# Kernel optimization log

Measured on AMD Instinct MI355X. Metric: run time of the kernel, lower is better.

## Reference

```python
import jax, jax.numpy as jnp
import numpy as np

# MLA (multi-head latent attention) config
DIM = 1024
HEADS = 16
DIM_HEAD = DIM // HEADS          # 64
LATENT = DIM // 4                # 256, compressed KV latent dim
SCALE = DIM_HEAD ** -0.5


def setup_inputs() -> dict:
    key = jax.random.key(0)
    ks = jax.random.split(key, 8)
    B, S = 2, 2048
    init = lambda k, shape, fan_in: jax.random.normal(k, shape, jnp.float32) * (fan_in ** -0.5)
    return {
        "x":  jax.random.normal(ks[0], (B, S, DIM), jnp.float32),
        "Wq": init(ks[1], (DIM, DIM), DIM),
        "bq": jnp.zeros((DIM,), jnp.float32),
        "Wl": init(ks[2], (DIM, LATENT), DIM),      # down-projection to compressed KV latent
        "bl": jnp.zeros((LATENT,), jnp.float32),
        "Wk": init(ks[3], (LATENT, DIM), LATENT),   # latent -> per-head keys
        "bk": jnp.zeros((DIM,), jnp.float32),
        "Wv": init(ks[4], (LATENT, DIM), LATENT),   # latent -> per-head values
        "bv": jnp.zeros((DIM,), jnp.float32),
        "Wo": init(ks[5], (DIM, DIM), DIM),         # Attention.to_out
        "bo": jnp.zeros((DIM,), jnp.float32),
    }


def reference(x, Wq, bq, Wl, bl, Wk, bk, Wv, bv, Wo, bo):
    B, S, D = x.shape
    H, Dh = HEADS, DIM_HEAD
    # query projection
    q = (x @ Wq + bq).reshape(B, S, H, Dh)
    # compressed KV latent (this is what would be cached; kv_cache=None here)
    latent = x @ Wl + bl                              # [B, S, LATENT]
    k = (latent @ Wk + bk).reshape(B, S, H, Dh)
    v = (latent @ Wv + bv).reshape(B, S, H, Dh)
    # attention
    scores = jnp.einsum('bihd,bjhd->bhij', q, k) * SCALE   # [B, H, S, S]
    attn = jax.nn.softmax(scores, axis=-1)
    out = jnp.einsum('bhij,bjhd->bihd', attn, v).reshape(B, S, D)
    # dropout(p=0) is identity; output projection
    out = out @ Wo + bo
    return out
```

## Files before the change

kernel.cpp:

```cpp
#include <hip/hip_runtime.h>


typedef _Float16 half8  __attribute__((ext_vector_type(8)));
typedef _Float16 half4  __attribute__((ext_vector_type(4)));
typedef float    floatx4 __attribute__((ext_vector_type(4)));

__global__ __launch_bounds__(256) void prep(
    const float* __restrict__ x,
    const float* __restrict__ Wq, const float* __restrict__ Wl,
    const float* __restrict__ Wk, const float* __restrict__ Wv,
    const float* __restrict__ Wo,
    _Float16* __restrict__ xh,
    _Float16* __restrict__ Bt1, _Float16* __restrict__ Bt2,
    _Float16* __restrict__ Wot)
{
    const int t = threadIdx.x;
    if (blockIdx.z == 5) {
        size_t base = ((size_t)(blockIdx.y * 32 + blockIdx.x) * 256 + t) * 16;
#pragma unroll
        for (int it = 0; it < 4; ++it) {
            floatx4 v = *(const floatx4*)(x + base + it * 4);
            *(half4*)(xh + base + it * 4) = __builtin_convertvector(v, half4);
        }
        return;
    }
    const float* src; _Float16* dst; int K, N;
    switch (blockIdx.z) {
        case 0:  src = Wq; dst = Bt1;                 K = 1024; N = 1024; break;
        case 1:  src = Wl; dst = Bt1 + 1024 * 1024;   K = 1024; N = 256;  break;
        case 2:  src = Wk; dst = Bt2;                 K = 256;  N = 1024; break;
        case 3:  src = Wv; dst = Bt2 + 1024 * 256;    K = 256;  N = 1024; break;
        default: src = Wo; dst = Wot;                 K = 1024; N = 1024; break;
    }
    const int n0 = blockIdx.x * 32, k0 = blockIdx.y * 32;
    if (n0 >= N || k0 >= K) return;
    __shared__ _Float16 tile[32][33];
    const int tx = t & 31, ty = t >> 5;
#pragma unroll
    for (int i = 0; i < 4; ++i)
        tile[ty + 8 * i][tx] = (_Float16)src[(size_t)(k0 + ty + 8 * i) * N + n0 + tx];
    __syncthreads();
#pragma unroll
    for (int i = 0; i < 4; ++i)
        dst[(size_t)(n0 + ty + 8 * i) * K + k0 + tx] = tile[tx][ty + 8 * i];
}

template <int MODE>
__global__ __launch_bounds__(256, 4) void gemm_fused(
    const _Float16* __restrict__ A, const _Float16* __restrict__ Bt,
    const float* __restrict__ bias0, const float* __restrict__ bias1,
    void* __restrict__ out0, void* __restrict__ out1,
    const _Float16* __restrict__ O1, const float* __restrict__ lp,
    int N, int K)
{
    __shared__ _Float16 As[128 * 32];
    __shared__ _Float16 Bs[64 * 32];
    __shared__ _Float16 Tt[(MODE == 1) ? 64 * 136 : 1];
    const int t = threadIdx.x;
    const int lane = t & 63, w = t >> 6;
    const int quad = lane >> 4, low = lane & 15;
    const int row0 = blockIdx.y * 128, col0 = blockIdx.x * 64;
    const int wm = (w >> 1) * 64, wn = (w & 1) * 32;

    floatx4 acc[4][2];
    const floatx4 z4 = {0.f, 0.f, 0.f, 0.f};
#pragma unroll
    for (int i = 0; i < 4; ++i)
#pragma unroll
        for (int j = 0; j < 2; ++j) acc[i][j] = z4;

    const int srow = lane >> 2;
    const int scol = (lane & 3) * 8;

    for (int k0 = 0; k0 < K; k0 += 32) {
        __syncthreads();
        if (MODE == 2) {
            const int head = k0 >> 6;
#pragma unroll
            for (int c = 0; c < 2; ++c) {
                const int chunk = w * 2 + c;
                const int row = row0 + chunk * 16 + srow;
                const int li = ((row >> 11) * 16 + head) * 2048 + (row & 2047);
                const float linv = 1.f / (lp[li] + lp[65536 + li]);
                const size_t gi = (size_t)row * 1024 + k0 + scol;
                half8 o0 = *(const half8*)(A + gi);
                half8 o1 = *(const half8*)(O1 + gi);
                half8 sm;
#pragma unroll
                for (int r = 0; r < 8; ++r)
                    sm[r] = (_Float16)(((float)o0[r] + (float)o1[r]) * linv);
                *(half8*)(As + chunk * 512 + lane * 8) = sm;
            }
        } else {
#pragma unroll
            for (int c = 0; c < 2; ++c) {
                const int chunk = w * 2 + c;
                const _Float16* g = A + (size_t)(row0 + chunk * 16 + srow) * K + k0 + scol;
                __builtin_amdgcn_global_load_lds(
                    (const __attribute__((address_space(1))) void*)g,
                    (__attribute__((address_space(3))) void*)(As + chunk * 512), 16, 0, 0);
            }
        }
        {
            const _Float16* g = Bt + (size_t)(col0 + w * 16 + srow) * K + k0 + scol;
            __builtin_amdgcn_global_load_lds(
                (const __attribute__((address_space(1))) void*)g,
                (__attribute__((address_space(3))) void*)(Bs + w * 512), 16, 0, 0);
        }
        __syncthreads();

        half8 a[4], b[2];
#pragma unroll
        for (int i = 0; i < 4; ++i)
            a[i] = *(const half8*)(As + (wm + i * 16 + low) * 32 + quad * 8);
#pragma unroll
        for (int j = 0; j < 2; ++j)
            b[j] = *(const half8*)(Bs + (wn + j * 16 + low) * 32 + quad * 8);
#pragma unroll
        for (int i = 0; i < 4; ++i)
#pragma unroll
            for (int j = 0; j < 2; ++j)
                acc[i][j] = __builtin_amdgcn_mfma_f32_16x16x32_f16(a[i], b[j], acc[i][j], 0, 0, 0);
    }

    if (MODE == 1 && col0 >= 1024) {
        const int hh = (col0 - 1024) >> 6;
        const int bb = row0 >> 11;
        const int tok0 = row0 & 2047;
#pragma unroll
        for (int i = 0; i < 4; ++i)
#pragma unroll
            for (int j = 0; j < 2; ++j) {
                const int lc = wn + j * 16 + low;
                float bv = bias1[hh * 64 + lc];
                half4 ph;
#pragma unroll
                for (int r = 0; r < 4; ++r) ph[r] = (_Float16)(acc[i][j][r] + bv);
                *(half4*)(&Tt[lc * 136 + wm + i * 16 + quad * 4]) = ph;
            }
        __syncthreads();
        _Float16* vb = (_Float16*)out1 + ((size_t)(bb * 16 + hh) * 64) * 2048;
#pragma unroll
        for (int it = 0; it < 4; ++it) {
            const int e = t + 256 * it;
            const int d = e >> 4, tk = (e & 15) * 8;
            half8 val = *(const half8*)(&Tt[d * 136 + tk]);
            *(half8*)(vb + (size_t)d * 2048 + tok0 + tk) = val;
        }
        return;
    }

#pragma unroll
    for (int i = 0; i < 4; ++i) {
#pragma unroll
        for (int j = 0; j < 2; ++j) {
            const int col = col0 + wn + j * 16 + low;
            const int rbase = row0 + wm + i * 16 + quad * 4;
            if (MODE == 2) {
                const float bv = bias0[col];
#pragma unroll
                for (int r = 0; r < 4; ++r)
                    ((float*)out0)[(size_t)(rbase + r) * 1024 + col] = acc[i][j][r] + bv;
            } else if (col < 1024) {
                float bv = bias0[col];
#pragma unroll
                for (int r = 0; r < 4; ++r) {
                    float val = acc[i][j][r] + bv;
                    if (MODE == 0) val *= 0.125f;
                    ((_Float16*)out0)[(size_t)(rbase + r) * 1024 + col] = (_Float16)val;
                }
            } else {
                const int c2 = col - 1024;
                float bv = bias1[c2];
#pragma unroll
                for (int r = 0; r < 4; ++r)
                    ((_Float16*)out1)[(size_t)(rbase + r) * 256 + c2] =
                        (_Float16)(acc[i][j][r] + bv);
            }
        }
    }
}

__global__ __launch_bounds__(256, 2) void mla_attn(
    const _Float16* __restrict__ qp,
    const _Float16* __restrict__ kk,
    const _Float16* __restrict__ vt,
    _Float16* __restrict__ Op0, _Float16* __restrict__ Op1,
    float* __restrict__ lp)
{
    constexpr int S = 2048;
    __shared__ _Float16 Ks[64][76];
    __shared__ _Float16 Vs[64][76];
    __shared__ _Float16 Ps[256][76];

    const int t = threadIdx.x, lane = t & 63, w = t >> 6;
    const int quad = lane >> 4, low = lane & 15;
    const int q0 = blockIdx.x * 256;
    const int b = blockIdx.y >> 4, h = blockIdx.y & 15;
    const int split = blockIdx.z;

    half8 qf[4][2];
#pragma unroll
    for (int ni = 0; ni < 4; ++ni)
#pragma unroll
        for (int ks = 0; ks < 2; ++ks)
            qf[ni][ks] = *(const half8*)(qp +
                (size_t)(b * S + q0 + w * 64 + ni * 16 + low) * 1024 +
                h * 64 + ks * 32 + quad * 8);

    floatx4 oa[4][4], ls[4];
    const floatx4 z4 = {0.f, 0.f, 0.f, 0.f};
#pragma unroll
    for (int mi = 0; mi < 4; ++mi) {
        ls[mi] = z4;
#pragma unroll
        for (int nd = 0; nd < 4; ++nd) oa[mi][nd] = z4;
    }

    const _Float16* kbase = kk + (size_t)(b * S) * 1024 + h * 64;
    const _Float16* vbase = vt + (size_t)(b * 16 + h) * 64 * 2048;

    const int jbeg = split * 1024, jend = jbeg + 1024;
    for (int j0 = jbeg; j0 < jend; j0 += 64) {
        __syncthreads();
#pragma unroll
        for (int p = 0; p < 2; ++p) {
            int c = p * 256 + t;
            int r = c >> 3, o8 = (c & 7) * 8;
            *(half8*)(&Ks[r][o8]) = *(const half8*)(kbase + (size_t)(j0 + r) * 1024 + o8);
            *(half8*)(&Vs[r][o8]) = *(const half8*)(vbase + (size_t)r * 2048 + j0 + o8);
        }
        __syncthreads();

        floatx4 s[4][4];
        const floatx4 i4 = {-3.f, -3.f, -3.f, -3.f};
#pragma unroll
        for (int mj = 0; mj < 4; ++mj)
#pragma unroll
            for (int ni = 0; ni < 4; ++ni) s[mj][ni] = i4;
#pragma unroll
        for (int ks = 0; ks < 2; ++ks) {
            half8 af[4];
#pragma unroll
            for (int mj = 0; mj < 4; ++mj)
                af[mj] = *(const half8*)(&Ks[mj * 16 + low][ks * 32 + quad * 8]);
#pragma unroll
            for (int mj = 0; mj < 4; ++mj)
#pragma unroll
                for (int ni = 0; ni < 4; ++ni)
                    s[mj][ni] = __builtin_amdgcn_mfma_f32_16x16x32_f16(af[mj], qf[ni][ks], s[mj][ni], 0, 0, 0);
        }

#pragma unroll
        for (int mj = 0; mj < 4; ++mj)
#pragma unroll
            for (int ni = 0; ni < 4; ++ni) {
                floatx4 pv;
#pragma unroll
                for (int r = 0; r < 4; ++r) pv[r] = __expf(s[mj][ni][r]);
                ls[ni] += pv;
                half4 ph;
#pragma unroll
                for (int r = 0; r < 4; ++r) ph[r] = (_Float16)pv[r];
                *(half4*)(&Ps[w * 64 + ni * 16 + low][mj * 16 + quad * 4]) = ph;
            }

#pragma unroll
        for (int ks = 0; ks < 2; ++ks) {
            half8 pf[4], vf[4];
#pragma unroll
            for (int mi = 0; mi < 4; ++mi)
                pf[mi] = *(const half8*)(&Ps[w * 64 + mi * 16 + low][ks * 32 + quad * 8]);
#pragma unroll
            for (int nd = 0; nd < 4; ++nd)
                vf[nd] = *(const half8*)(&Vs[nd * 16 + low][ks * 32 + quad * 8]);
#pragma unroll
            for (int mi = 0; mi < 4; ++mi)
#pragma unroll
                for (int nd = 0; nd < 4; ++nd)
                    oa[mi][nd] = __builtin_amdgcn_mfma_f32_16x16x32_f16(pf[mi], vf[nd], oa[mi][nd], 0, 0, 0);
        }
    }

#pragma unroll
    for (int ni = 0; ni < 4; ++ni) {
        float l = ls[ni][0] + ls[ni][1] + ls[ni][2] + ls[ni][3];
        l += __shfl_xor(l, 16);
        l += __shfl_xor(l, 32);
        if (quad == 0)
            lp[split * 65536 + (b * 16 + h) * 2048 + q0 + w * 64 + ni * 16 + low] = l;
    }
    _Float16* op = split ? Op1 : Op0;
#pragma unroll
    for (int mi = 0; mi < 4; ++mi)
#pragma unroll
        for (int nd = 0; nd < 4; ++nd)
#pragma unroll
            for (int r = 0; r < 4; ++r)
                op[(size_t)(b * S + q0 + w * 64 + mi * 16 + quad * 4 + r) * 1024 +
                   h * 64 + nd * 16 + low] = (_Float16)oa[mi][nd][r];
}

extern "C" void kernel_launch(void* const* d_in, const int* in_sizes, int n_in,
                              void* d_out, int out_size, void* d_ws, size_t ws_size,
                              hipStream_t stream) {
    const float* x  = (const float*)d_in[0];
    const float* Wq = (const float*)d_in[1];
    const float* bq = (const float*)d_in[2];
    const float* Wl = (const float*)d_in[3];
    const float* bl = (const float*)d_in[4];
    const float* Wk = (const float*)d_in[5];
    const float* bk = (const float*)d_in[6];
    const float* Wv = (const float*)d_in[7];
    const float* bv = (const float*)d_in[8];
    const float* Wo = (const float*)d_in[9];
    const float* bo = (const float*)d_in[10];
    float* out = (float*)d_out;

    _Float16* p   = (_Float16*)d_ws;
    _Float16* xh  = p; p += 4194304;
    _Float16* qh  = p; p += 4194304;
    _Float16* kh  = p; p += 4194304;
    _Float16* vtb = p; p += 4194304;
    _Float16* ah  = p; p += 4194304;
    _Float16* lat = p; p += 1048576;
    _Float16* Bt1 = p; p += 1310720;
    _Float16* Bt2 = p; p += 524288;
    _Float16* Wot = p; p += 1048576;

    prep<<<dim3(32, 32, 6), 256, 0, stream>>>(x, Wq, Wl, Wk, Wv, Wo, xh, Bt1, Bt2, Wot);

    gemm_fused<0><<<dim3(20, 32), 256, 0, stream>>>(
        xh, Bt1, bq, bl, qh, lat, nullptr, nullptr, 1280, 1024);
    gemm_fused<1><<<dim3(32, 32), 256, 0, stream>>>(
        lat, Bt2, bk, bv, kh, vtb, nullptr, nullptr, 2048, 256);
    mla_attn<<<dim3(8, 32, 2), 256, 0, stream>>>(qh, kh, vtb, ah, xh, (float*)lat);
    gemm_fused<2><<<dim3(16, 32), 256, 0, stream>>>(
        ah, Wot, bo, nullptr, out, nullptr, xh, (const float*)lat, 1024, 1024);
}
```

Before: 226.2 us.

## Swizzle GEMM operand layouts in global memory and split attention combine into its own kernel

```diff
diff --git a/kernel.cpp b/kernel.cpp
--- a/kernel.cpp
+++ b/kernel.cpp
@@ -4,6 +4,8 @@
 typedef _Float16 half8  __attribute__((ext_vector_type(8)));
 typedef _Float16 half4  __attribute__((ext_vector_type(4)));
 typedef float    floatx4 __attribute__((ext_vector_type(4)));
+
+__device__ __forceinline__ int swz_mask(int row) { return ((row ^ (row >> 2)) & 3) << 3; }
 
 __global__ __launch_bounds__(256) void prep(
     const float* __restrict__ x,
@@ -16,11 +18,16 @@
 {
     const int t = threadIdx.x;
     if (blockIdx.z == 5) {
-        size_t base = ((size_t)(blockIdx.y * 32 + blockIdx.x) * 256 + t) * 16;
+        size_t gbase = ((size_t)(blockIdx.y * 32 + blockIdx.x) * 256 + t) * 16;
+        const int row = (int)(gbase >> 10);
+        const int m = swz_mask(row);
+        const size_t rowbase = (size_t)row << 10;
+        const int h0 = (int)(gbase & 1023);
 #pragma unroll
         for (int it = 0; it < 4; ++it) {
-            floatx4 v = *(const floatx4*)(x + base + it * 4);
-            *(half4*)(xh + base + it * 4) = __builtin_convertvector(v, half4);
+            floatx4 v = *(const floatx4*)(x + gbase + it * 4);
+            *(half4*)(xh + rowbase + ((h0 + it * 4) ^ m)) =
+                __builtin_convertvector(v, half4);
         }
         return;
     }
@@ -41,8 +48,10 @@
         tile[ty + 8 * i][tx] = (_Float16)src[(size_t)(k0 + ty + 8 * i) * N + n0 + tx];
     __syncthreads();
 #pragma unroll
-    for (int i = 0; i < 4; ++i)
-        dst[(size_t)(n0 + ty + 8 * i) * K + k0 + tx] = tile[tx][ty + 8 * i];
+    for (int i = 0; i < 4; ++i) {
+        const int n = n0 + ty + 8 * i;
+        dst[(size_t)n * K + ((k0 + tx) ^ swz_mask(n))] = tile[tx][ty + 8 * i];
+    }
 }
 
 template <int MODE>
@@ -50,7 +59,6 @@
     const _Float16* __restrict__ A, const _Float16* __restrict__ Bt,
     const float* __restrict__ bias0, const float* __restrict__ bias1,
     void* __restrict__ out0, void* __restrict__ out1,
-    const _Float16* __restrict__ O1, const float* __restrict__ lp,
     int N, int K)
 {
     __shared__ _Float16 As[128 * 32];
@@ -61,6 +69,7 @@
     const int quad = lane >> 4, low = lane & 15;
     const int row0 = blockIdx.y * 128, col0 = blockIdx.x * 64;
     const int wm = (w >> 1) * 64, wn = (w & 1) * 32;
+    const int swz = ((low ^ (low >> 2)) & 3) << 3;
 
     floatx4 acc[4][2];
     const floatx4 z4 = {0.f, 0.f, 0.f, 0.f};
@@ -74,32 +83,13 @@
 
     for (int k0 = 0; k0 < K; k0 += 32) {
         __syncthreads();
-        if (MODE == 2) {
-            const int head = k0 >> 6;
-#pragma unroll
-            for (int c = 0; c < 2; ++c) {
-                const int chunk = w * 2 + c;
-                const int row = row0 + chunk * 16 + srow;
-                const int li = ((row >> 11) * 16 + head) * 2048 + (row & 2047);
-                const float linv = 1.f / (lp[li] + lp[65536 + li]);
-                const size_t gi = (size_t)row * 1024 + k0 + scol;
-                half8 o0 = *(const half8*)(A + gi);
-                half8 o1 = *(const half8*)(O1 + gi);
-                half8 sm;
-#pragma unroll
-                for (int r = 0; r < 8; ++r)
-                    sm[r] = (_Float16)(((float)o0[r] + (float)o1[r]) * linv);
-                *(half8*)(As + chunk * 512 + lane * 8) = sm;
-            }
-        } else {
-#pragma unroll
-            for (int c = 0; c < 2; ++c) {
-                const int chunk = w * 2 + c;
-                const _Float16* g = A + (size_t)(row0 + chunk * 16 + srow) * K + k0 + scol;
-                __builtin_amdgcn_global_load_lds(
-                    (const __attribute__((address_space(1))) void*)g,
-                    (__attribute__((address_space(3))) void*)(As + chunk * 512), 16, 0, 0);
-            }
+#pragma unroll
+        for (int c = 0; c < 2; ++c) {
+            const int chunk = w * 2 + c;
+            const _Float16* g = A + (size_t)(row0 + chunk * 16 + srow) * K + k0 + scol;
+            __builtin_amdgcn_global_load_lds(
+                (const __attribute__((address_space(1))) void*)g,
+                (__attribute__((address_space(3))) void*)(As + chunk * 512), 16, 0, 0);
         }
         {
             const _Float16* g = Bt + (size_t)(col0 + w * 16 + srow) * K + k0 + scol;
@@ -112,10 +102,10 @@
         half8 a[4], b[2];
 #pragma unroll
         for (int i = 0; i < 4; ++i)
-            a[i] = *(const half8*)(As + (wm + i * 16 + low) * 32 + quad * 8);
+            a[i] = *(const half8*)(As + (wm + i * 16 + low) * 32 + ((quad * 8) ^ swz));
 #pragma unroll
         for (int j = 0; j < 2; ++j)
-            b[j] = *(const half8*)(Bs + (wn + j * 16 + low) * 32 + quad * 8);
+            b[j] = *(const half8*)(Bs + (wn + j * 16 + low) * 32 + ((quad * 8) ^ swz));
 #pragma unroll
         for (int i = 0; i < 4; ++i)
 #pragma unroll
@@ -173,9 +163,11 @@
                 const int c2 = col - 1024;
                 float bv = bias1[c2];
 #pragma unroll
-                for (int r = 0; r < 4; ++r)
-                    ((_Float16*)out1)[(size_t)(rbase + r) * 256 + c2] =
+                for (int r = 0; r < 4; ++r) {
+                    const int row = rbase + r;
+                    ((_Float16*)out1)[(size_t)row * 256 + (c2 ^ swz_mask(row))] =
                         (_Float16)(acc[i][j][r] + bv);
+                }
             }
         }
     }
@@ -299,6 +291,24 @@
             for (int r = 0; r < 4; ++r)
                 op[(size_t)(b * S + q0 + w * 64 + mi * 16 + quad * 4 + r) * 1024 +
                    h * 64 + nd * 16 + low] = (_Float16)oa[mi][nd][r];
+}
+
+__global__ __launch_bounds__(256) void attn_combine(
+    const _Float16* __restrict__ O0, const _Float16* __restrict__ O1,
+    const float* __restrict__ lp, _Float16* __restrict__ att)
+{
+    size_t idx = ((size_t)blockIdx.x * 256 + threadIdx.x) * 8;
+    int row = (int)(idx >> 10), c = (int)(idx & 1023);
+    int b = row >> 11, qq = row & 2047, h = c >> 6;
+    int li = (b * 16 + h) * 2048 + qq;
+    float inv = 1.f / (lp[li] + lp[65536 + li]);
+    half8 a = *(const half8*)(O0 + idx);
+    half8 bb = *(const half8*)(O1 + idx);
+    half8 o;
+#pragma unroll
+    for (int r = 0; r < 8; ++r)
+        o[r] = (_Float16)(((float)a[r] + (float)bb[r]) * inv);
+    *(half8*)(att + ((size_t)row << 10) + (c ^ swz_mask(row))) = o;
 }
 
 extern "C" void kernel_launch(void* const* d_in, const int* in_sizes, int n_in,
@@ -331,10 +341,11 @@
     prep<<<dim3(32, 32, 6), 256, 0, stream>>>(x, Wq, Wl, Wk, Wv, Wo, xh, Bt1, Bt2, Wot);
 
     gemm_fused<0><<<dim3(20, 32), 256, 0, stream>>>(
-        xh, Bt1, bq, bl, qh, lat, nullptr, nullptr, 1280, 1024);
+        xh, Bt1, bq, bl, qh, lat, 1280, 1024);
     gemm_fused<1><<<dim3(32, 32), 256, 0, stream>>>(
-        lat, Bt2, bk, bv, kh, vtb, nullptr, nullptr, 2048, 256);
+        lat, Bt2, bk, bv, kh, vtb, 2048, 256);
     mla_attn<<<dim3(8, 32, 2), 256, 0, stream>>>(qh, kh, vtb, ah, xh, (float*)lat);
+    attn_combine<<<2048, 256, 0, stream>>>(ah, xh, (const float*)lat, kh);
     gemm_fused<2><<<dim3(16, 32), 256, 0, stream>>>(
-        ah, Wot, bo, nullptr, out, nullptr, xh, (const float*)lat, 1024, 1024);
-}
+        kh, Wot, bo, nullptr, out, nullptr, 1024, 1024);
+}
```

Result: faster. 210.7 us (-6.9%).
